# Kernel tuning notes

Measured on AMD Instinct MI355X. Metric: run time of the kernel, lower is better.

The kernel has to match this reference:

```python
import jax, jax.numpy as jnp
import numpy as np

B, S, I, H = 64, 512, 1024, 1024

def setup_inputs() -> dict:
    key = jax.random.key(0)
    ks = jax.random.split(key, 5)
    sqrt_k = 1.0 / np.sqrt(H)
    return {
        "sequence": jax.random.normal(ks[0], (B, S, I), dtype=jnp.float32),
        "hidden_state": jnp.zeros((B, H), dtype=jnp.float32),
        "w_ih": jax.random.uniform(ks[1], (H, I), dtype=jnp.float32, minval=-sqrt_k, maxval=sqrt_k),
        "w_hh": jax.random.uniform(ks[2], (H, H), dtype=jnp.float32, minval=-sqrt_k, maxval=sqrt_k),
        "b_ih": jax.random.uniform(ks[3], (H,), dtype=jnp.float32, minval=-sqrt_k, maxval=sqrt_k),
        "b_hh": jax.random.uniform(ks[4], (H,), dtype=jnp.float32, minval=-sqrt_k, maxval=sqrt_k),
    }

def reference(sequence, hidden_state, w_ih, w_hh, b_ih, b_hh):
    # Precompute the input projection for all timesteps in one big GEMM:
    # x_proj[b,s,h] = sequence[b,s,:] @ w_ih.T + b_ih
    x_proj = jnp.einsum('bsi,hi->bsh', sequence, w_ih) + b_ih

    def step(h, x_t):
        # h_new = relu(x_t + h @ w_hh.T + b_hh)  -- Elman recurrence
        h_new = jax.nn.relu(x_t + jnp.einsum('bh,gh->bg', h, w_hh) + b_hh)
        return h_new, h_new

    # scan over time (leading axis)
    h_last, outs = jax.lax.scan(step, hidden_state, jnp.swapaxes(x_proj, 0, 1))
    output = jnp.swapaxes(outs, 0, 1)  # [B, S, H]
    return output, h_last
```

## Files before the change

### kernel.cpp

```cpp
#include <hip/hip_runtime.h>
#include <hip/hip_bf16.h>

#define B_SZ  64
#define S_LEN 512
#define I_DIM 1024
#define H_DIM 1024

typedef __bf16 bf16x8 __attribute__((ext_vector_type(8)));
typedef __bf16 bf16x4 __attribute__((ext_vector_type(4)));
typedef float  f32x4  __attribute__((ext_vector_type(4)));
typedef unsigned u32x4 __attribute__((ext_vector_type(4)));

#define MFMA16(a,b,c) __builtin_amdgcn_mfma_f32_16x16x32_bf16((a),(b),(c),0,0,0)

__device__ inline bf16x8 cvt8(const float4& a, const float4& b) {
  bf16x8 v;
  v[0]=(__bf16)a.x; v[1]=(__bf16)a.y; v[2]=(__bf16)a.z; v[3]=(__bf16)a.w;
  v[4]=(__bf16)b.x; v[5]=(__bf16)b.y; v[6]=(__bf16)b.z; v[7]=(__bf16)b.w;
  return v;
}
__device__ inline bf16x8 cvt8v(const f32x4& a, const f32x4& b) {
  bf16x8 v;
  v[0]=(__bf16)a[0]; v[1]=(__bf16)a[1]; v[2]=(__bf16)a[2]; v[3]=(__bf16)a[3];
  v[4]=(__bf16)b[0]; v[5]=(__bf16)b[1]; v[6]=(__bf16)b[2]; v[7]=(__bf16)b[3];
  return v;
}

__device__ inline u32x4 load_b128_sc(const void* p) {
  u32x4 r;
  asm volatile("global_load_dwordx4 %0, %1, off sc0 sc1"
               : "=v"(r) : "v"(p) : "memory");
  return r;
}
__device__ inline void store_b64_sc(void* p, unsigned long long v) {
  asm volatile("global_store_dwordx2 %0, %1, off sc0 sc1"
               :: "v"(p), "v"(v) : "memory");
}
__device__ inline f32x4 load_b128_pf(const void* p) {
  f32x4 r;
  asm volatile("global_load_dwordx4 %0, %1, off"
               : "=v"(r) : "v"(p) : "memory");
  return r;
}
__device__ inline void waitcnt_vm0() { asm volatile("s_waitcnt vmcnt(0)" ::: "memory"); }

__global__ void k_hinit(const float* __restrict__ h0, __bf16* __restrict__ hbuf) {
  const int i = blockIdx.x * 256 + threadIdx.x;
  const float4 v = ((const float4*)h0)[i];
  __bf16* p = hbuf + (size_t)i * 4;
  p[0] = (__bf16)v.x; p[1] = (__bf16)v.y; p[2] = (__bf16)v.z; p[3] = (__bf16)v.w;
}

#define P1_LDA 40
__global__ __launch_bounds__(256, 2) void k_xproj(
    const float* __restrict__ A, const float* __restrict__ W,
    const float* __restrict__ bias, float* __restrict__ C) {
  constexpr int K = I_DIM, N = H_DIM;
  __shared__ __bf16 As[128][P1_LDA];
  __shared__ __bf16 Bs[128][P1_LDA];
  const int bid = blockIdx.x;
  const int nt = bid & 7, mt = bid >> 3;
  const int m0 = mt * 128, n0 = nt * 128;
  const int tid = threadIdx.x, lane = tid & 63, wv = tid >> 6;
  const int wm = (wv & 1) * 64, wn = (wv >> 1) * 64;
  const int fr = lane & 15, fq = lane >> 4;
  const int srow = tid >> 1, scol = (tid & 1) * 16;
  const float* gA = A + (size_t)(m0 + srow) * K + scol;
  const float* gB = W + (size_t)(n0 + srow) * K + scol;
  const f32x4 zero = {0.f, 0.f, 0.f, 0.f};
  f32x4 acc[4][4];
  #pragma unroll
  for (int m = 0; m < 4; ++m)
    #pragma unroll
    for (int n = 0; n < 4; ++n) acc[m][n] = zero;

  for (int k0 = 0; k0 < K; k0 += 32) {
    float4 a0 = *(const float4*)(gA + k0);
    float4 a1 = *(const float4*)(gA + k0 + 4);
    float4 a2 = *(const float4*)(gA + k0 + 8);
    float4 a3 = *(const float4*)(gA + k0 + 12);
    float4 b0 = *(const float4*)(gB + k0);
    float4 b1 = *(const float4*)(gB + k0 + 4);
    float4 b2 = *(const float4*)(gB + k0 + 8);
    float4 b3 = *(const float4*)(gB + k0 + 12);
    __syncthreads();
    *(bf16x8*)(&As[srow][scol])     = cvt8(a0, a1);
    *(bf16x8*)(&As[srow][scol + 8]) = cvt8(a2, a3);
    *(bf16x8*)(&Bs[srow][scol])     = cvt8(b0, b1);
    *(bf16x8*)(&Bs[srow][scol + 8]) = cvt8(b2, b3);
    __syncthreads();
    bf16x8 af[4], bfr[4];
    #pragma unroll
    for (int m = 0; m < 4; ++m) af[m]  = *(const bf16x8*)(&As[wm + m*16 + fr][fq*8]);
    #pragma unroll
    for (int n = 0; n < 4; ++n) bfr[n] = *(const bf16x8*)(&Bs[wn + n*16 + fr][fq*8]);
    #pragma unroll
    for (int m = 0; m < 4; ++m)
      #pragma unroll
      for (int n = 0; n < 4; ++n)
        acc[m][n] = MFMA16(af[m], bfr[n], acc[m][n]);
  }
  #pragma unroll
  for (int n = 0; n < 4; ++n) {
    const int col = n0 + wn + n*16 + fr;
    const float bv = bias[col];
    #pragma unroll
    for (int m = 0; m < 4; ++m) {
      const int row = m0 + wm + m*16 + fq*4;
      #pragma unroll
      for (int jj = 0; jj < 4; ++jj)
        C[(size_t)(row + jj) * N + col] = acc[m][n][jj] + bv;
    }
  }
}

#define NGR 4
#define BG  16
#define WPG 16
#define RPW 64

__global__ __launch_bounds__(256, 1) void k_rnn(
    const float* __restrict__ w_hh, const float* __restrict__ b_hh,
    float* __restrict__ out, __bf16* __restrict__ hbuf,
    unsigned* __restrict__ ctrs)
{
  __shared__ __bf16 Hs[BG][H_DIM];
  const int bid = blockIdx.x;
  const int g = bid >> 4, j = bid & 15;
  const int r0 = j * RPW;
  const int tid = threadIdx.x, lane = tid & 63, wv = tid >> 6;
  const int fr = lane & 15, fq = lane >> 4;
  const int myW  = r0 + wv * 16 + fr;
  const int row4 = r0 + wv * 16 + fq * 4;
  const int b    = g * BG + fr;
  const int hswz = (fr & 7) << 3;

  bf16x8 wfrag[32];
  {
    const float* wsrc = w_hh + (size_t)myW * H_DIM + fq * 8;
    #pragma unroll
    for (int kk = 0; kk < 32; ++kk) {
      f32x4 w0 = *(const f32x4*)(wsrc + kk * 32);
      f32x4 w1 = *(const f32x4*)(wsrc + kk * 32 + 4);
      wfrag[kk] = cvt8v(w0, w1);
    }
  }
  const f32x4 bh = *(const f32x4*)(b_hh + row4);
  unsigned* ctr = ctrs + (g << 6);
  const size_t BH  = (size_t)B_SZ * H_DIM;
  const size_t bsh = (size_t)B_SZ * S_LEN * H_DIM;
  const __bf16* hg0 = hbuf + (size_t)g * BG * H_DIM;

  size_t xo = (size_t)b * S_LEN * H_DIM + row4;
  f32x4 xv = load_b128_pf(out + xo);

  for (int t = 0; t < S_LEN; ++t) {
    const __bf16* hsrc = hg0 + (size_t)(t & 1) * BH;
    u32x4 st[8];
    #pragma unroll
    for (int i = 0; i < 8; ++i) {
      const int c = tid + (i << 8);
      st[i] = load_b128_sc(hsrc + c * 8);
    }
    waitcnt_vm0();
    asm volatile("" : "+v"(xv));
    #pragma unroll
    for (int i = 0; i < 8; ++i) {
      const int c = tid + (i << 8);
      const int bb = c >> 7, k = (c & 127) << 3;
      *(u32x4*)&Hs[bb][k ^ ((bb & 7) << 3)] = st[i];
    }
    __syncthreads();

    const f32x4 z = {0.f, 0.f, 0.f, 0.f};
    f32x4 a0 = z, a1 = z, a2 = z, a3 = z;
    #pragma unroll
    for (int kk = 0; kk < 32; kk += 4) {
      bf16x8 h0 = *(const bf16x8*)&Hs[fr][((kk + 0) * 32 + fq * 8) ^ hswz];
      a0 = MFMA16(wfrag[kk + 0], h0, a0);
      bf16x8 h1 = *(const bf16x8*)&Hs[fr][((kk + 1) * 32 + fq * 8) ^ hswz];
      a1 = MFMA16(wfrag[kk + 1], h1, a1);
      bf16x8 h2 = *(const bf16x8*)&Hs[fr][((kk + 2) * 32 + fq * 8) ^ hswz];
      a2 = MFMA16(wfrag[kk + 2], h2, a2);
      bf16x8 h3 = *(const bf16x8*)&Hs[fr][((kk + 3) * 32 + fq * 8) ^ hswz];
      a3 = MFMA16(wfrag[kk + 3], h3, a3);
    }

    f32x4 s = (a0 + a1) + (a2 + a3);
    f32x4 r;
    r[0] = fmaxf(xv[0] + s[0] + bh[0], 0.f);
    r[1] = fmaxf(xv[1] + s[1] + bh[1], 0.f);
    r[2] = fmaxf(xv[2] + s[2] + bh[2], 0.f);
    r[3] = fmaxf(xv[3] + s[3] + bh[3], 0.f);
    *(f32x4*)(out + xo) = r;
    if (t == S_LEN - 1)
      *(f32x4*)(out + bsh + (size_t)b * H_DIM + row4) = r;
    bf16x4 hv;
    hv[0] = (__bf16)r[0]; hv[1] = (__bf16)r[1];
    hv[2] = (__bf16)r[2]; hv[3] = (__bf16)r[3];
    __bf16* hdst = hbuf + (size_t)((t + 1) & 1) * BH + (size_t)b * H_DIM + row4;
    store_b64_sc(hdst, __builtin_bit_cast(unsigned long long, hv));

    waitcnt_vm0();
    __syncthreads();
    if (tid == 0)
      __hip_atomic_fetch_add(ctr, 1u, __ATOMIC_RELAXED, __HIP_MEMORY_SCOPE_AGENT);
    xo += H_DIM;
    xv = load_b128_pf(out + xo);
    if (tid == 0) {
      const unsigned tgt = (unsigned)(t + 1) * WPG;
      while (__hip_atomic_load(ctr, __ATOMIC_RELAXED, __HIP_MEMORY_SCOPE_AGENT) < tgt)
        __builtin_amdgcn_s_sleep(1);
    }
    __syncthreads();
  }
}

extern "C" void kernel_launch(void* const* d_in, const int* in_sizes, int n_in,
                              void* d_out, int out_size, void* d_ws, size_t ws_size,
                              hipStream_t stream) {
  const float* seq  = (const float*)d_in[0];
  const float* h0   = (const float*)d_in[1];
  const float* w_ih = (const float*)d_in[2];
  const float* w_hh = (const float*)d_in[3];
  const float* b_ih = (const float*)d_in[4];
  const float* b_hh = (const float*)d_in[5];
  float* out = (float*)d_out;

  __bf16* hbuf = (__bf16*)d_ws;
  unsigned* ctrs = (unsigned*)((char*)d_ws + (size_t)2 * B_SZ * H_DIM * sizeof(__bf16));

  hipMemsetAsync(ctrs, 0, NGR * 64 * sizeof(unsigned), stream);
  k_hinit<<<dim3(B_SZ * H_DIM / 4 / 256), dim3(256), 0, stream>>>(h0, hbuf);
  k_xproj<<<dim3((B_SZ * S_LEN / 128) * (H_DIM / 128)), dim3(256), 0, stream>>>(
      seq, w_ih, b_ih, out);

  const float* a0 = w_hh; const float* a1 = b_hh; float* a2 = out;
  __bf16* a3 = hbuf; unsigned* a4 = ctrs;
  void* args[5] = { &a0, &a1, &a2, &a3, &a4 };
  hipLaunchCooperativeKernel((void*)k_rnn, dim3(NGR * WPG), dim3(256),
                             args, 0, stream);
}
```

Baseline: 1.660 ms.

## Replace atomic-counter barrier with per-chunk timestep flags and use 512-thread blocks

The recurrent kernel no longer uses a per-group atomic counter and spin barrier. Each hidden-state chunk is now stored as a 16-byte record that carries its timestep tag, and readers poll each chunk until the tag matches the current step. This removes the global barrier round-trip from the critical path of every step. Blocks grow to 512 threads covering 128 rows each, halving the number of blocks per group to 8. The cost is doubled bytes per hidden-state exchange and repeated polling loads.

```diff
diff --git a/kernel.cpp b/kernel.cpp
--- a/kernel.cpp
+++ b/kernel.cpp
@@ -32,8 +32,8 @@
                : "=v"(r) : "v"(p) : "memory");
   return r;
 }
-__device__ inline void store_b64_sc(void* p, unsigned long long v) {
-  asm volatile("global_store_dwordx2 %0, %1, off sc0 sc1"
+__device__ inline void store_b128_sc(void* p, u32x4 v) {
+  asm volatile("global_store_dwordx4 %0, %1, off sc0 sc1"
                :: "v"(p), "v"(v) : "memory");
 }
 __device__ inline f32x4 load_b128_pf(const void* p) {
@@ -44,11 +44,18 @@
 }
 __device__ inline void waitcnt_vm0() { asm volatile("s_waitcnt vmcnt(0)" ::: "memory"); }
 
-__global__ void k_hinit(const float* __restrict__ h0, __bf16* __restrict__ hbuf) {
-  const int i = blockIdx.x * 256 + threadIdx.x;
-  const float4 v = ((const float4*)h0)[i];
-  __bf16* p = hbuf + (size_t)i * 4;
-  p[0] = (__bf16)v.x; p[1] = (__bf16)v.y; p[2] = (__bf16)v.z; p[3] = (__bf16)v.w;
+__global__ void k_hinit(const float* __restrict__ h0, u32x4* __restrict__ chunks) {
+  const int ci = blockIdx.x * 256 + threadIdx.x;
+  const float4 v = ((const float4*)h0)[ci];
+  bf16x4 hv;
+  hv[0] = (__bf16)v.x; hv[1] = (__bf16)v.y; hv[2] = (__bf16)v.z; hv[3] = (__bf16)v.w;
+  const unsigned long long h64 = __builtin_bit_cast(unsigned long long, hv);
+  u32x4 pk;
+  pk[0] = (unsigned)h64; pk[1] = (unsigned)(h64 >> 32); pk[2] = 0u; pk[3] = 0u;
+  store_b128_sc(chunks + ci, pk);
+  u32x4 inv;
+  inv[0] = 0u; inv[1] = 0u; inv[2] = 0xFFFFFFFFu; inv[3] = 0u;
+  store_b128_sc(chunks + 16384 + ci, inv);
 }
 
 #define P1_LDA 40
@@ -116,17 +123,17 @@
 
 #define NGR 4
 #define BG  16
-#define WPG 16
-#define RPW 64
-
-__global__ __launch_bounds__(256, 1) void k_rnn(
+#define WPG 8
+#define RPW 128
+#define CPB (B_SZ * 256)
+
+__global__ __launch_bounds__(512, 1) void k_rnn(
     const float* __restrict__ w_hh, const float* __restrict__ b_hh,
-    float* __restrict__ out, __bf16* __restrict__ hbuf,
-    unsigned* __restrict__ ctrs)
+    float* __restrict__ out, u32x4* __restrict__ chunks)
 {
   __shared__ __bf16 Hs[BG][H_DIM];
   const int bid = blockIdx.x;
-  const int g = bid >> 4, j = bid & 15;
+  const int g = bid >> 3, j = bid & 7;
   const int r0 = j * RPW;
   const int tid = threadIdx.x, lane = tid & 63, wv = tid >> 6;
   const int fr = lane & 15, fq = lane >> 4;
@@ -146,30 +153,35 @@
     }
   }
   const f32x4 bh = *(const f32x4*)(b_hh + row4);
-  unsigned* ctr = ctrs + (g << 6);
-  const size_t BH  = (size_t)B_SZ * H_DIM;
   const size_t bsh = (size_t)B_SZ * S_LEN * H_DIM;
-  const __bf16* hg0 = hbuf + (size_t)g * BG * H_DIM;
+  const u32x4* gsrc0 = chunks + (size_t)g * (BG * 256);
+  const size_t mysto = (size_t)b * 256 + (row4 >> 2);
 
   size_t xo = (size_t)b * S_LEN * H_DIM + row4;
   f32x4 xv = load_b128_pf(out + xo);
 
   for (int t = 0; t < S_LEN; ++t) {
-    const __bf16* hsrc = hg0 + (size_t)(t & 1) * BH;
-    u32x4 st[8];
-    #pragma unroll
-    for (int i = 0; i < 8; ++i) {
-      const int c = tid + (i << 8);
-      st[i] = load_b128_sc(hsrc + c * 8);
-    }
-    waitcnt_vm0();
-    asm volatile("" : "+v"(xv));
-    #pragma unroll
-    for (int i = 0; i < 8; ++i) {
-      const int c = tid + (i << 8);
-      const int bb = c >> 7, k = (c & 127) << 3;
-      *(u32x4*)&Hs[bb][k ^ ((bb & 7) << 3)] = st[i];
-    }
+    const u32x4* src = gsrc0 + (size_t)(t & 1) * CPB;
+    unsigned pend = 0xFF;
+    do {
+      u32x4 st[8];
+      #pragma unroll
+      for (int i = 0; i < 8; ++i)
+        if (pend & (1u << i)) st[i] = load_b128_sc(src + tid + (i << 9));
+      waitcnt_vm0();
+      #pragma unroll
+      for (int i = 0; i < 8; ++i)
+        if (pend & (1u << i)) {
+          if (st[i][2] == (unsigned)t) {
+            const int bb = (i << 1) + (tid >> 8);
+            const int k4 = tid & 255;
+            const unsigned long long d =
+                ((unsigned long long)st[i][1] << 32) | st[i][0];
+            *(unsigned long long*)&Hs[bb][(k4 << 2) ^ ((bb & 7) << 3)] = d;
+            pend &= ~(1u << i);
+          }
+        }
+    } while (pend);
     __syncthreads();
 
     const f32x4 z = {0.f, 0.f, 0.f, 0.f};
@@ -198,20 +210,14 @@
     bf16x4 hv;
     hv[0] = (__bf16)r[0]; hv[1] = (__bf16)r[1];
     hv[2] = (__bf16)r[2]; hv[3] = (__bf16)r[3];
-    __bf16* hdst = hbuf + (size_t)((t + 1) & 1) * BH + (size_t)b * H_DIM + row4;
-    store_b64_sc(hdst, __builtin_bit_cast(unsigned long long, hv));
-
-    waitcnt_vm0();
-    __syncthreads();
-    if (tid == 0)
-      __hip_atomic_fetch_add(ctr, 1u, __ATOMIC_RELAXED, __HIP_MEMORY_SCOPE_AGENT);
+    const unsigned long long h64 = __builtin_bit_cast(unsigned long long, hv);
+    u32x4 pk;
+    pk[0] = (unsigned)h64; pk[1] = (unsigned)(h64 >> 32);
+    pk[2] = (unsigned)(t + 1); pk[3] = 0u;
+    store_b128_sc((void*)(chunks + (size_t)((t + 1) & 1) * CPB + mysto), pk);
+
     xo += H_DIM;
     xv = load_b128_pf(out + xo);
-    if (tid == 0) {
-      const unsigned tgt = (unsigned)(t + 1) * WPG;
-      while (__hip_atomic_load(ctr, __ATOMIC_RELAXED, __HIP_MEMORY_SCOPE_AGENT) < tgt)
-        __builtin_amdgcn_s_sleep(1);
-    }
     __syncthreads();
   }
 }
@@ -227,17 +233,15 @@
   const float* b_hh = (const float*)d_in[5];
   float* out = (float*)d_out;
 
-  __bf16* hbuf = (__bf16*)d_ws;
-  unsigned* ctrs = (unsigned*)((char*)d_ws + (size_t)2 * B_SZ * H_DIM * sizeof(__bf16));
-
-  hipMemsetAsync(ctrs, 0, NGR * 64 * sizeof(unsigned), stream);
-  k_hinit<<<dim3(B_SZ * H_DIM / 4 / 256), dim3(256), 0, stream>>>(h0, hbuf);
+  u32x4* chunks = (u32x4*)d_ws;
+
+  k_hinit<<<dim3(CPB / 256), dim3(256), 0, stream>>>(h0, chunks);
   k_xproj<<<dim3((B_SZ * S_LEN / 128) * (H_DIM / 128)), dim3(256), 0, stream>>>(
       seq, w_ih, b_ih, out);
 
   const float* a0 = w_hh; const float* a1 = b_hh; float* a2 = out;
-  __bf16* a3 = hbuf; unsigned* a4 = ctrs;
-  void* args[5] = { &a0, &a1, &a2, &a3, &a4 };
-  hipLaunchCooperativeKernel((void*)k_rnn, dim3(NGR * WPG), dim3(256),
+  u32x4* a3 = chunks;
+  void* args[4] = { &a0, &a1, &a2, &a3 };
+  hipLaunchCooperativeKernel((void*)k_rnn, dim3(NGR * WPG), dim3(512),
                              args, 0, stream);
 }
```

Result: slower. 2.104 ms (+26.8%).

## Replace atomic counter barrier with per-wave flags and larger recurrent workgroups

Applied to the files above, without the earlier changes.

The recurrent kernel now uses 512-thread blocks (8 waves) covering 128 hidden rows each, halving the workgroups per batch group to 8. The shared atomic counter, block-wide syncthreads and single-thread spin are replaced by per-wave step flags: each wave publishes its step number with a coherent store, and every wave polls all 64 flags of its group in one vector load before reading the hidden state. Flag zeroing moves into the init kernel, which drops the memset launch. This targets per-step synchronization latency, which dominates the serial 512-step scan, at the cost of many more polling loads and fewer, larger workgroups.

```diff
diff --git a/kernel.cpp b/kernel.cpp
--- a/kernel.cpp
+++ b/kernel.cpp
@@ -5,6 +5,7 @@
 #define S_LEN 512
 #define I_DIM 1024
 #define H_DIM 1024
+#define BH    (B_SZ * H_DIM)
 
 typedef __bf16 bf16x8 __attribute__((ext_vector_type(8)));
 typedef __bf16 bf16x4 __attribute__((ext_vector_type(4)));
@@ -32,7 +33,7 @@
                : "=v"(r) : "v"(p) : "memory");
   return r;
 }
-__device__ inline void store_b64_sc(void* p, unsigned long long v) {
+__device__ inline void st64_sc(void* p, unsigned long long v) {
   asm volatile("global_store_dwordx2 %0, %1, off sc0 sc1"
                :: "v"(p), "v"(v) : "memory");
 }
@@ -42,13 +43,22 @@
                : "=v"(r) : "v"(p) : "memory");
   return r;
 }
-__device__ inline void waitcnt_vm0() { asm volatile("s_waitcnt vmcnt(0)" ::: "memory"); }
-
-__global__ void k_hinit(const float* __restrict__ h0, __bf16* __restrict__ hbuf) {
-  const int i = blockIdx.x * 256 + threadIdx.x;
-  const float4 v = ((const float4*)h0)[i];
-  __bf16* p = hbuf + (size_t)i * 4;
-  p[0] = (__bf16)v.x; p[1] = (__bf16)v.y; p[2] = (__bf16)v.z; p[3] = (__bf16)v.w;
+__device__ inline void waitcnt_vm0() {
+  asm volatile("s_waitcnt vmcnt(0)" ::: "memory");
+}
+
+__global__ void k_hinit(const float* __restrict__ h0, __bf16* __restrict__ ht,
+                        unsigned* __restrict__ flags) {
+  const int ci = blockIdx.x * 256 + threadIdx.x;
+  const float4 v = ((const float4*)h0)[ci];
+  bf16x4 hv;
+  hv[0] = (__bf16)v.x; hv[1] = (__bf16)v.y; hv[2] = (__bf16)v.z; hv[3] = (__bf16)v.w;
+  st64_sc(ht + (size_t)ci * 4, __builtin_bit_cast(unsigned long long, hv));
+  if (blockIdx.x == 0) {
+    unsigned z = 0u;
+    asm volatile("global_store_dword %0, %1, off sc0 sc1"
+                 :: "v"(flags + threadIdx.x), "v"(z) : "memory");
+  }
 }
 
 #define P1_LDA 40
@@ -116,18 +126,17 @@
 
 #define NGR 4
 #define BG  16
-#define WPG 16
-#define RPW 64
-
-__global__ __launch_bounds__(256, 1) void k_rnn(
+#define WPG 8
+
+__global__ __launch_bounds__(512, 1) void k_rnn(
     const float* __restrict__ w_hh, const float* __restrict__ b_hh,
-    float* __restrict__ out, __bf16* __restrict__ hbuf,
-    unsigned* __restrict__ ctrs)
+    float* __restrict__ out, __bf16* __restrict__ ht,
+    unsigned* __restrict__ flags)
 {
   __shared__ __bf16 Hs[BG][H_DIM];
   const int bid = blockIdx.x;
-  const int g = bid >> 4, j = bid & 15;
-  const int r0 = j * RPW;
+  const int g = bid >> 3, j = bid & 7;
+  const int r0 = j * 128;
   const int tid = threadIdx.x, lane = tid & 63, wv = tid >> 6;
   const int fr = lane & 15, fq = lane >> 4;
   const int myW  = r0 + wv * 16 + fr;
@@ -146,27 +155,37 @@
     }
   }
   const f32x4 bh = *(const f32x4*)(b_hh + row4);
-  unsigned* ctr = ctrs + (g << 6);
-  const size_t BH  = (size_t)B_SZ * H_DIM;
   const size_t bsh = (size_t)B_SZ * S_LEN * H_DIM;
-  const __bf16* hg0 = hbuf + (size_t)g * BG * H_DIM;
+  const __bf16* hg0 = ht + (size_t)g * BG * H_DIM;
+  const unsigned* fp = flags + (g << 6) + lane;
+  unsigned* myfp = flags + (g << 6) + (j << 3) + wv;
 
   size_t xo = (size_t)b * S_LEN * H_DIM + row4;
   f32x4 xv = load_b128_pf(out + xo);
 
   for (int t = 0; t < S_LEN; ++t) {
+    if (t) {
+      const unsigned tt = (unsigned)t;
+      for (;;) {
+        unsigned f;
+        asm volatile("global_load_dword %0, %1, off sc0 sc1"
+                     : "=v"(f) : "v"(fp) : "memory");
+        waitcnt_vm0();
+        __builtin_amdgcn_sched_barrier(0);
+        if (__all((int)(f >= tt))) break;
+      }
+    }
+
     const __bf16* hsrc = hg0 + (size_t)(t & 1) * BH;
-    u32x4 st[8];
-    #pragma unroll
-    for (int i = 0; i < 8; ++i) {
-      const int c = tid + (i << 8);
-      st[i] = load_b128_sc(hsrc + c * 8);
-    }
+    u32x4 st[4];
+    #pragma unroll
+    for (int i = 0; i < 4; ++i)
+      st[i] = load_b128_sc(hsrc + (size_t)(tid + (i << 9)) * 8);
     waitcnt_vm0();
-    asm volatile("" : "+v"(xv));
-    #pragma unroll
-    for (int i = 0; i < 8; ++i) {
-      const int c = tid + (i << 8);
+    __builtin_amdgcn_sched_barrier(0);
+    #pragma unroll
+    for (int i = 0; i < 4; ++i) {
+      const int c = tid + (i << 9);
       const int bb = c >> 7, k = (c & 127) << 3;
       *(u32x4*)&Hs[bb][k ^ ((bb & 7) << 3)] = st[i];
     }
@@ -198,20 +217,17 @@
     bf16x4 hv;
     hv[0] = (__bf16)r[0]; hv[1] = (__bf16)r[1];
     hv[2] = (__bf16)r[2]; hv[3] = (__bf16)r[3];
-    __bf16* hdst = hbuf + (size_t)((t + 1) & 1) * BH + (size_t)b * H_DIM + row4;
-    store_b64_sc(hdst, __builtin_bit_cast(unsigned long long, hv));
+    __bf16* hd = ht + (size_t)((t + 1) & 1) * BH + (size_t)b * H_DIM + row4;
+    st64_sc(hd, __builtin_bit_cast(unsigned long long, hv));
 
     waitcnt_vm0();
-    __syncthreads();
-    if (tid == 0)
-      __hip_atomic_fetch_add(ctr, 1u, __ATOMIC_RELAXED, __HIP_MEMORY_SCOPE_AGENT);
+    if (lane == 0) {
+      unsigned tv = (unsigned)(t + 1);
+      asm volatile("global_store_dword %0, %1, off sc0 sc1"
+                   :: "v"(myfp), "v"(tv) : "memory");
+    }
     xo += H_DIM;
     xv = load_b128_pf(out + xo);
-    if (tid == 0) {
-      const unsigned tgt = (unsigned)(t + 1) * WPG;
-      while (__hip_atomic_load(ctr, __ATOMIC_RELAXED, __HIP_MEMORY_SCOPE_AGENT) < tgt)
-        __builtin_amdgcn_s_sleep(1);
-    }
     __syncthreads();
   }
 }
@@ -227,17 +243,16 @@
   const float* b_hh = (const float*)d_in[5];
   float* out = (float*)d_out;
 
-  __bf16* hbuf = (__bf16*)d_ws;
-  unsigned* ctrs = (unsigned*)((char*)d_ws + (size_t)2 * B_SZ * H_DIM * sizeof(__bf16));
-
-  hipMemsetAsync(ctrs, 0, NGR * 64 * sizeof(unsigned), stream);
-  k_hinit<<<dim3(B_SZ * H_DIM / 4 / 256), dim3(256), 0, stream>>>(h0, hbuf);
+  __bf16* ht = (__bf16*)d_ws;
+  unsigned* flags = (unsigned*)((char*)d_ws + (size_t)2 * BH * sizeof(__bf16));
+
+  k_hinit<<<dim3(BH / 4 / 256), dim3(256), 0, stream>>>(h0, ht, flags);
   k_xproj<<<dim3((B_SZ * S_LEN / 128) * (H_DIM / 128)), dim3(256), 0, stream>>>(
       seq, w_ih, b_ih, out);
 
   const float* a0 = w_hh; const float* a1 = b_hh; float* a2 = out;
-  __bf16* a3 = hbuf; unsigned* a4 = ctrs;
+  __bf16* a3 = ht; unsigned* a4 = flags;
   void* args[5] = { &a0, &a1, &a2, &a3, &a4 };
-  hipLaunchCooperativeKernel((void*)k_rnn, dim3(NGR * WPG), dim3(256),
+  hipLaunchCooperativeKernel((void*)k_rnn, dim3(NGR * WPG), dim3(512),
                              args, 0, stream);
 }
```

Measured after the change: 1.964 ms. 18.3% more time.
